# Kernel tuning notes

Measured on AMD Instinct MI355X. Metric: run time of the kernel, lower is better.

## Reference

```python
import jax, jax.numpy as jnp
import numpy as np

FILTER_SIZES = [3, 5, 7, 11, 15, 23, 37, 55]
NB_GROUP = 8
CHAN = 512
IN_CHAN = 3


def setup_inputs() -> dict:
    key = jax.random.key(0)
    keys = jax.random.split(key, 2 + 2 * len(FILTER_SIZES))
    B, H, W = 2, 128, 128
    cpf = CHAN // len(FILTER_SIZES)  # 64 channels per filter size
    inp = {"x": jax.random.normal(keys[0], (B, IN_CHAN, H, W), jnp.float32)}
    for i, k in enumerate(FILTER_SIZES):
        fan_in = IN_CHAN * k * k
        inp[f"w{i}"] = jax.random.normal(keys[1 + 2 * i], (cpf, IN_CHAN, k, k), jnp.float32) / np.sqrt(fan_in).astype(np.float32)
        inp[f"b{i}"] = 0.01 * jax.random.normal(keys[2 + 2 * i], (cpf,), jnp.float32)
    # torch.randperm channel shuffle, fixed for determinism
    inp["perm"] = jax.random.permutation(keys[-1], CHAN)
    return inp


def _conv_relu(x, w, b, k):
    p = (k - 1) // 2  # same padding (odd filter sizes)
    y = jax.lax.conv_general_dilated(
        x, w, window_strides=(1, 1), padding=[(p, p), (p, p)],
        dimension_numbers=("NCHW", "OIHW", "NCHW"))
    return jax.nn.relu(y + b[None, :, None, None])


def reference(x, w0, b0, w1, b1, w2, b2, w3, b3, w4, b4, w5, b5, w6, b6, w7, b7, perm):
    ws = [w0, w1, w2, w3, w4, w5, w6, w7]
    bs = [b0, b1, b2, b3, b4, b5, b6, b7]
    feats = [_conv_relu(x, ws[i], bs[i], FILTER_SIZES[i]) for i in range(len(FILTER_SIZES))]
    feat = jnp.concatenate(feats, axis=1)          # [B, 512, H, W]
    feat = feat[:, perm]                            # channel shuffle
    B, C, H, W = feat.shape
    g = NB_GROUP
    s = C // g
    # unfold(1,s,s)+permute(0,1,4,2,3) == reshape to [B, g, s, H, W]
    feat = feat.reshape(B * g, s, H * W)            # [B*g, s, HW]
    # graham order 2: (feat[:, :, None] * feat[:, None, :]).sum(-1) as a contraction
    gram = jnp.einsum("bcn,bdn->bcd", feat, feat)  # [B*g, s, s]
    return gram.reshape(B, g, s * s)                # [B, g, s*s]
```

## Files before the change

### kernel.cpp

```cpp
#include <hip/hip_runtime.h>
#include <hip/hip_bf16.h>
#include <cstdint>

typedef __attribute__((ext_vector_type(8))) short short8;
typedef __attribute__((ext_vector_type(4))) short short4v;
typedef __attribute__((ext_vector_type(4))) float f32x4;
typedef __attribute__((ext_vector_type(16))) float f32x16;

static constexpr int HWPIX = 16384;
static constexpr int NCH   = 512;
static constexpr int GCHK  = 32;

__device__ __forceinline__ unsigned short f2bf(float f) {
    unsigned int u = __float_as_uint(f);
    u = (u + 0x7fffu + ((u >> 16) & 1u)) >> 16;
    return (unsigned short)u;
}

template<int K> struct KG {
    static constexpr int P       = (K - 1) / 2;
    static constexpr int NSEC    = (K + 7) / 8;
    static constexpr int SEGS    = 3 * K;
    static constexpr int NCHK16  = (SEGS + 1) / 2;
    static constexpr int NCHKP16 = ((NCHK16 + 3) / 4) * 4;
    static constexpr int COLS    = 128 + K - 1;
    static constexpr int XPAD    = 128;
    static constexpr int XSE     = COLS * 24 + XPAD;
};
static_assert(3048 + KG< 3>::NCHKP16 * 16 <= KG< 3>::XSE, "pad3");
static_assert(3048 + KG< 5>::NCHKP16 * 16 <= KG< 5>::XSE, "pad5");
static_assert(3048 + KG< 7>::NCHKP16 * 16 <= KG< 7>::XSE, "pad7");
static_assert(3048 + KG<11>::NCHKP16 * 16 <= KG<11>::XSE, "pad11");
static_assert(3048 + KG<15>::NCHKP16 * 16 <= KG<15>::XSE, "pad15");
static_assert(3048 + KG<23>::NCHKP16 * 16 <= KG<23>::XSE, "pad23");
static_assert(3048 + KG<37>::NCHKP16 * 16 <= KG<37>::XSE, "pad37");
static_assert(3048 + KG<55>::NCHKP16 * 16 <= KG<55>::XSE, "pad55");
static_assert(2 * KG<55>::XSE * 2 <= 33792, "dbuf fits smem");

struct PtrArgs {
    const float* w[8];
    const float* bias[8];
    unsigned short* wpk[8];
    int cum[9];
};

template<int K>
__device__ void repack_body(const float* __restrict__ w, unsigned short* __restrict__ wpk, int t) {
    constexpr int NCHKP16 = KG<K>::NCHKP16;
    const int sec = t / NCHKP16;
    const int t16 = t - sec * NCHKP16;
    const int tid = threadIdx.x;
    if (tid >= 128) return;
    const int strip = tid >> 6;
    const int lane  = tid & 63;
    const int co    = strip * 32 + (lane & 31);
    const int seg   = 2 * t16 + (lane >> 5);
    int kw = 0, r = 0;
    const bool vseg = seg < KG<K>::SEGS;
    if (vseg) { kw = seg / 3; r = seg - kw * 3; }
    short8 o;
    #pragma unroll
    for (int j = 0; j < 8; ++j) {
        const int icr = r * 8 + j;
        const int ic  = icr >> 3;
        const int kh  = sec * 8 + (icr & 7);
        float v = 0.f;
        if (vseg && kh < K)
            v = w[((co * 3 + ic) * K + kh) * K + kw];
        o[j] = (short)f2bf(v);
    }
    *reinterpret_cast<short8*>(wpk + ((size_t)t * 128 + strip * 64 + lane) * 8) = o;
}

__global__ __launch_bounds__(256) void repack_all(PtrArgs a) {
    const int blk = blockIdx.x;
    int f = 0;
    #pragma unroll
    for (int i = 0; i < 8; ++i) if (blk >= a.cum[i + 1]) f = i + 1;
    const int t = blk - a.cum[f];
    switch (f) {
        case 0: repack_body< 3>(a.w[0], a.wpk[0], t); break;
        case 1: repack_body< 5>(a.w[1], a.wpk[1], t); break;
        case 2: repack_body< 7>(a.w[2], a.wpk[2], t); break;
        case 3: repack_body<11>(a.w[3], a.wpk[3], t); break;
        case 4: repack_body<15>(a.w[4], a.wpk[4], t); break;
        case 5: repack_body<23>(a.w[5], a.wpk[5], t); break;
        case 6: repack_body<37>(a.w[6], a.wpk[6], t); break;
        case 7: repack_body<55>(a.w[7], a.wpk[7], t); break;
    }
}

#define MFMA32 __builtin_amdgcn_mfma_f32_32x32x16_bf16

template<int K>
__device__ void conv_body(const float* __restrict__ x, const unsigned short* __restrict__ wpk,
                          const float* __restrict__ bias, unsigned short* __restrict__ feat,
                          int cbase, char* smem, int bx)
{
    constexpr int P        = KG<K>::P;
    constexpr int NCHKP16  = KG<K>::NCHKP16;
    constexpr int NSEC     = KG<K>::NSEC;
    constexpr int COLS     = KG<K>::COLS;
    constexpr int XSE      = KG<K>::XSE;

    unsigned short* xs0 = (unsigned short*)smem;
    float* red = (float*)smem;

    const int tid = threadIdx.x;
    const int b   = bx >> 7;
    const int h   = bx & 127;

    const int lane = tid & 63;
    const int wv   = tid >> 6;
    const int l31  = lane & 31;
    const int lh   = lane >> 5;

    const float* xb = x + (size_t)b * 3 * HWPIX;

    for (int i = tid * 4; i < KG<K>::XPAD; i += 1024) {
        *reinterpret_cast<short4v*>(xs0 + COLS * 24 + i)       = short4v{0, 0, 0, 0};
        *reinterpret_cast<short4v*>(xs0 + XSE + COLS * 24 + i) = short4v{0, 0, 0, 0};
    }

    auto stage = [&](int sec, unsigned short* dst) {
        for (int e = tid * 4; e < 24 * COLS; e += 1024) {
            const int c  = e / 24;
            const int i0 = e - c * 24;
            const int col = c - P;
            short4v pk;
            #pragma unroll
            for (int j = 0; j < 4; ++j) {
                const int icr = i0 + j;
                const int ic  = icr >> 3;
                const int row = h + sec * 8 + (icr & 7) - P;
                float v = 0.f;
                if ((unsigned)row < 128u && (unsigned)col < 128u)
                    v = xb[ic * HWPIX + row * 128 + col];
                pk[j] = (short)f2bf(v);
            }
            *reinterpret_cast<short4v*>(dst + e) = pk;
        }
    };

    stage(0, xs0);
    __syncthreads();

    f32x16 acc[2][4] = {};

    for (int s = 0; s < NSEC; ++s) {
        if (s + 1 < NSEC) stage(s + 1, xs0 + ((s + 1) & 1) * XSE);

        const unsigned short* xsR  = xs0 + (s & 1) * XSE;
        const unsigned short* wsec = wpk + (size_t)s * NCHKP16 * 1024 + lane * 8;

        for (int tt = 0; tt < NCHKP16 / 4; ++tt) {
            const int t16 = tt * 4 + wv;
            const unsigned short* ap = wsec + (size_t)t16 * 1024;
            short8 a0 = *reinterpret_cast<const short8*>(ap);
            short8 a1 = *reinterpret_cast<const short8*>(ap + 512);
            const unsigned short* bp = xsR + l31 * 24 + lh * 8 + t16 * 16;
            short8 b0 = *reinterpret_cast<const short8*>(bp);
            short8 b1 = *reinterpret_cast<const short8*>(bp + 768);
            short8 b2 = *reinterpret_cast<const short8*>(bp + 1536);
            short8 b3 = *reinterpret_cast<const short8*>(bp + 2304);

            acc[0][0] = MFMA32(a0, b0, acc[0][0], 0, 0, 0);
            acc[0][1] = MFMA32(a0, b1, acc[0][1], 0, 0, 0);
            acc[0][2] = MFMA32(a0, b2, acc[0][2], 0, 0, 0);
            acc[0][3] = MFMA32(a0, b3, acc[0][3], 0, 0, 0);
            acc[1][0] = MFMA32(a1, b0, acc[1][0], 0, 0, 0);
            acc[1][1] = MFMA32(a1, b1, acc[1][1], 0, 0, 0);
            acc[1][2] = MFMA32(a1, b2, acc[1][2], 0, 0, 0);
            acc[1][3] = MFMA32(a1, b3, acc[1][3], 0, 0, 0);
        }
        __syncthreads();
    }

    const float bv  = bias[tid >> 2];
    const int   eco = tid >> 2;
    const int   px8 = (tid & 3) * 8;
    const size_t fbase = (((size_t)(b * NCH + cbase + eco)) << 14) + h * 128;

    #pragma unroll
    for (int q = 0; q < 4; ++q) {
        if (q > 0) __syncthreads();
        #pragma unroll
        for (int strip = 0; strip < 2; ++strip)
            #pragma unroll
            for (int reg = 0; reg < 16; ++reg) {
                const int co = strip * 32 + (reg & 3) + 8 * (reg >> 2) + 4 * lh;
                red[(wv * 64 + co) * 33 + l31] = acc[strip][q][reg];
            }
        __syncthreads();
        short8 o;
        #pragma unroll
        for (int j = 0; j < 8; ++j) {
            const int px = px8 + j;
            float v = red[(0 * 64 + eco) * 33 + px] + red[(1 * 64 + eco) * 33 + px]
                    + red[(2 * 64 + eco) * 33 + px] + red[(3 * 64 + eco) * 33 + px];
            o[j] = (short)f2bf(fmaxf(v + bv, 0.f));
        }
        *reinterpret_cast<short8*>(feat + fbase + q * 32 + px8) = o;
    }
}

__global__ __launch_bounds__(256, 2) void conv_all(const float* __restrict__ x,
                                                   PtrArgs a, unsigned short* __restrict__ feat)
{
    __shared__ __align__(16) char smem[33792];
    switch (7 - blockIdx.y) {
        case 0: conv_body< 3>(x, a.wpk[0], a.bias[0], feat, 0 * 64, smem, blockIdx.x); break;
        case 1: conv_body< 5>(x, a.wpk[1], a.bias[1], feat, 1 * 64, smem, blockIdx.x); break;
        case 2: conv_body< 7>(x, a.wpk[2], a.bias[2], feat, 2 * 64, smem, blockIdx.x); break;
        case 3: conv_body<11>(x, a.wpk[3], a.bias[3], feat, 3 * 64, smem, blockIdx.x); break;
        case 4: conv_body<15>(x, a.wpk[4], a.bias[4], feat, 4 * 64, smem, blockIdx.x); break;
        case 5: conv_body<23>(x, a.wpk[5], a.bias[5], feat, 5 * 64, smem, blockIdx.x); break;
        case 6: conv_body<37>(x, a.wpk[6], a.bias[6], feat, 6 * 64, smem, blockIdx.x); break;
        case 7: conv_body<55>(x, a.wpk[7], a.bias[7], feat, 7 * 64, smem, blockIdx.x); break;
    }
}

#define MFMA_BF16 __builtin_amdgcn_mfma_f32_16x16x32_bf16

__global__ __launch_bounds__(256) void gram_mfma(
    const unsigned short* __restrict__ feat, const int* __restrict__ perm,
    float* __restrict__ part)
{
    __shared__ __align__(16) unsigned short tile[64 * 256];
    __shared__ int permch[64];

    const int bg = blockIdx.y, chunk = blockIdx.x;
    const int b = bg >> 3, gq = bg & 7;
    const int tid = threadIdx.x;

    if (tid < 64) permch[tid] = perm[gq * 64 + tid];
    __syncthreads();

    const int lane = tid & 63;
    const int wv   = tid >> 6;
    const int ln15 = lane & 15;
    const int kg   = lane >> 4;

    f32x4 acc[4] = {};
    const size_t pxbase = (size_t)chunk * 512;

    for (int p2 = 0; p2 < 2; ++p2) {
        {
            const int r0 = tid >> 5;
            const int g  = tid & 31;
            #pragma unroll
            for (int it = 0; it < 8; ++it) {
                const int r = it * 8 + r0;
                const unsigned short* src =
                    feat + (((size_t)(b * NCH + permch[r])) << 14) + pxbase + p2 * 256 + g * 8;
                short8 v = *reinterpret_cast<const short8*>(src);
                *reinterpret_cast<short8*>(tile + r * 256 + ((g ^ (r & 7)) * 8)) = v;
            }
        }
        __syncthreads();
        #pragma unroll
        for (int t = 0; t < 8; ++t) {
            const int g  = t * 4 + kg;
            const int ra = wv * 16 + ln15;
            short8 av = *reinterpret_cast<const short8*>(tile + ra * 256 + ((g ^ (ra & 7)) * 8));
            #pragma unroll
            for (int cs = 0; cs < 4; ++cs) {
                const int rb = cs * 16 + ln15;
                short8 bv = *reinterpret_cast<const short8*>(tile + rb * 256 + ((g ^ (rb & 7)) * 8));
                acc[cs] = MFMA_BF16(av, bv, acc[cs], 0, 0, 0);
            }
        }
        __syncthreads();
    }

    float* pp = part + ((size_t)bg * GCHK + chunk) * 4096;
    #pragma unroll
    for (int cs = 0; cs < 4; ++cs)
        #pragma unroll
        for (int i = 0; i < 4; ++i) {
            const int row = wv * 16 + kg * 4 + i;
            const int col = cs * 16 + ln15;
            pp[row * 64 + col] = acc[cs][i];
        }
}

__global__ __launch_bounds__(256) void gram_reduce(
    const float* __restrict__ part, float* __restrict__ out)
{
    const int idx = blockIdx.x * 256 + threadIdx.x;
    const int bg  = idx >> 12;
    const int e   = idx & 4095;
    const float* p = part + (size_t)bg * GCHK * 4096 + e;
    float s = 0.f;
    #pragma unroll
    for (int c = 0; c < GCHK; ++c) s += p[c * 4096];
    out[idx] = s;
}

extern "C" void kernel_launch(void* const* d_in, const int* in_sizes, int n_in,
                              void* d_out, int out_size, void* d_ws, size_t ws_size,
                              hipStream_t stream) {
    const float* x = (const float*)d_in[0];
    const int* perm = (const int*)d_in[17];

    unsigned short* feat = (unsigned short*)d_ws;
    float* part = (float*)((char*)d_ws + (size_t)2 * NCH * HWPIX * sizeof(unsigned short));
    unsigned short* wpk0 = (unsigned short*)((char*)part + (size_t)16 * GCHK * 4096 * sizeof(float));
    float* out = (float*)d_out;

    const int nchk[8] = { KG<3>::NSEC * KG<3>::NCHKP16,  KG<5>::NSEC * KG<5>::NCHKP16,
                          KG<7>::NSEC * KG<7>::NCHKP16,  KG<11>::NSEC * KG<11>::NCHKP16,
                          KG<15>::NSEC * KG<15>::NCHKP16, KG<23>::NSEC * KG<23>::NCHKP16,
                          KG<37>::NSEC * KG<37>::NCHKP16, KG<55>::NSEC * KG<55>::NCHKP16 };
    PtrArgs a;
    int acc = 0;
    for (int i = 0; i < 8; ++i) {
        a.w[i]    = (const float*)d_in[1 + 2 * i];
        a.bias[i] = (const float*)d_in[2 + 2 * i];
        a.wpk[i]  = wpk0 + (size_t)acc * 1024;
        a.cum[i]  = acc;
        acc += nchk[i];
    }
    a.cum[8] = acc;

    repack_all<<<acc, 256, 0, stream>>>(a);
    conv_all<<<dim3(256, 8), 256, 0, stream>>>(x, a, feat);
    gram_mfma<<<dim3(GCHK, 16), 256, 0, stream>>>(feat, perm, part);
    gram_reduce<<<dim3(65536 / 256), 256, 0, stream>>>(part, out);
}
```

Measured before the change: 105.8 us.

## Give each wave private input sections instead of splitting chunks across waves

```diff
diff --git a/kernel.cpp b/kernel.cpp
--- a/kernel.cpp
+++ b/kernel.cpp
@@ -27,15 +27,16 @@
     static constexpr int XPAD    = 128;
     static constexpr int XSE     = COLS * 24 + XPAD;
 };
-static_assert(3048 + KG< 3>::NCHKP16 * 16 <= KG< 3>::XSE, "pad3");
-static_assert(3048 + KG< 5>::NCHKP16 * 16 <= KG< 5>::XSE, "pad5");
-static_assert(3048 + KG< 7>::NCHKP16 * 16 <= KG< 7>::XSE, "pad7");
-static_assert(3048 + KG<11>::NCHKP16 * 16 <= KG<11>::XSE, "pad11");
-static_assert(3048 + KG<15>::NCHKP16 * 16 <= KG<15>::XSE, "pad15");
-static_assert(3048 + KG<23>::NCHKP16 * 16 <= KG<23>::XSE, "pad23");
-static_assert(3048 + KG<37>::NCHKP16 * 16 <= KG<37>::XSE, "pad37");
-static_assert(3048 + KG<55>::NCHKP16 * 16 <= KG<55>::XSE, "pad55");
-static_assert(2 * KG<55>::XSE * 2 <= 33792, "dbuf fits smem");
+static_assert(3048 + KG< 3>::NCHK16 * 16 <= KG< 3>::XSE, "pad3");
+static_assert(3048 + KG< 5>::NCHK16 * 16 <= KG< 5>::XSE, "pad5");
+static_assert(3048 + KG< 7>::NCHK16 * 16 <= KG< 7>::XSE, "pad7");
+static_assert(3048 + KG<11>::NCHK16 * 16 <= KG<11>::XSE, "pad11");
+static_assert(3048 + KG<15>::NCHK16 * 16 <= KG<15>::XSE, "pad15");
+static_assert(3048 + KG<23>::NCHK16 * 16 <= KG<23>::XSE, "pad23");
+static_assert(3048 + KG<37>::NCHK16 * 16 <= KG<37>::XSE, "pad37");
+static_assert(3048 + KG<55>::NCHK16 * 16 <= KG<55>::XSE, "pad55");
+static_assert(4 * KG<55>::XSE * 2 <= 35968, "4 wave buffers fit smem");
+static_assert(256 * 33 * 4 <= 35968, "red fits smem");
 
 struct PtrArgs {
     const float* w[8];
@@ -98,14 +99,12 @@
                           int cbase, char* smem, int bx)
 {
     constexpr int P        = KG<K>::P;
+    constexpr int NCHK16   = KG<K>::NCHK16;
     constexpr int NCHKP16  = KG<K>::NCHKP16;
     constexpr int NSEC     = KG<K>::NSEC;
     constexpr int COLS     = KG<K>::COLS;
     constexpr int XSE      = KG<K>::XSE;
 
-    unsigned short* xs0 = (unsigned short*)smem;
-    float* red = (float*)smem;
-
     const int tid = threadIdx.x;
     const int b   = bx >> 7;
     const int h   = bx & 127;
@@ -115,15 +114,18 @@
     const int l31  = lane & 31;
     const int lh   = lane >> 5;
 
+    unsigned short* xs = (unsigned short*)smem + wv * XSE;
+    float* red = (float*)smem;
+
     const float* xb = x + (size_t)b * 3 * HWPIX;
 
-    for (int i = tid * 4; i < KG<K>::XPAD; i += 1024) {
-        *reinterpret_cast<short4v*>(xs0 + COLS * 24 + i)       = short4v{0, 0, 0, 0};
-        *reinterpret_cast<short4v*>(xs0 + XSE + COLS * 24 + i) = short4v{0, 0, 0, 0};
-    }
-
-    auto stage = [&](int sec, unsigned short* dst) {
-        for (int e = tid * 4; e < 24 * COLS; e += 1024) {
+    for (int i = lane * 4; i < KG<K>::XPAD; i += 256)
+        *reinterpret_cast<short4v*>(xs + COLS * 24 + i) = short4v{0, 0, 0, 0};
+
+    f32x16 acc[2][4] = {};
+
+    for (int s = wv; s < NSEC; s += 4) {
+        for (int e = lane * 4; e < 24 * COLS; e += 256) {
             const int c  = e / 24;
             const int i0 = e - c * 24;
             const int col = c - P;
@@ -132,33 +134,21 @@
             for (int j = 0; j < 4; ++j) {
                 const int icr = i0 + j;
                 const int ic  = icr >> 3;
-                const int row = h + sec * 8 + (icr & 7) - P;
+                const int row = h + s * 8 + (icr & 7) - P;
                 float v = 0.f;
                 if ((unsigned)row < 128u && (unsigned)col < 128u)
                     v = xb[ic * HWPIX + row * 128 + col];
                 pk[j] = (short)f2bf(v);
             }
-            *reinterpret_cast<short4v*>(dst + e) = pk;
-        }
-    };
-
-    stage(0, xs0);
-    __syncthreads();
-
-    f32x16 acc[2][4] = {};
-
-    for (int s = 0; s < NSEC; ++s) {
-        if (s + 1 < NSEC) stage(s + 1, xs0 + ((s + 1) & 1) * XSE);
-
-        const unsigned short* xsR  = xs0 + (s & 1) * XSE;
+            *reinterpret_cast<short4v*>(xs + e) = pk;
+        }
+
         const unsigned short* wsec = wpk + (size_t)s * NCHKP16 * 1024 + lane * 8;
-
-        for (int tt = 0; tt < NCHKP16 / 4; ++tt) {
-            const int t16 = tt * 4 + wv;
+        for (int t16 = 0; t16 < NCHK16; ++t16) {
             const unsigned short* ap = wsec + (size_t)t16 * 1024;
             short8 a0 = *reinterpret_cast<const short8*>(ap);
             short8 a1 = *reinterpret_cast<const short8*>(ap + 512);
-            const unsigned short* bp = xsR + l31 * 24 + lh * 8 + t16 * 16;
+            const unsigned short* bp = xs + l31 * 24 + lh * 8 + t16 * 16;
             short8 b0 = *reinterpret_cast<const short8*>(bp);
             short8 b1 = *reinterpret_cast<const short8*>(bp + 768);
             short8 b2 = *reinterpret_cast<const short8*>(bp + 1536);
@@ -173,9 +163,9 @@
             acc[1][2] = MFMA32(a1, b2, acc[1][2], 0, 0, 0);
             acc[1][3] = MFMA32(a1, b3, acc[1][3], 0, 0, 0);
         }
-        __syncthreads();
-    }
-
+    }
+
+    __syncthreads();
     const float bv  = bias[tid >> 2];
     const int   eco = tid >> 2;
     const int   px8 = (tid & 3) * 8;
@@ -207,7 +197,7 @@
 __global__ __launch_bounds__(256, 2) void conv_all(const float* __restrict__ x,
                                                    PtrArgs a, unsigned short* __restrict__ feat)
 {
-    __shared__ __align__(16) char smem[33792];
+    __shared__ __align__(16) char smem[35968];
     switch (7 - blockIdx.y) {
         case 0: conv_body< 3>(x, a.wpk[0], a.bias[0], feat, 0 * 64, smem, blockIdx.x); break;
         case 1: conv_body< 5>(x, a.wpk[1], a.bias[1], feat, 1 * 64, smem, blockIdx.x); break;
```

Result: slower. 123.0 us (+16.2%).

## Stream conv weight tiles into LDS via async global_load_lds double buffering

Applied to the files above, without the earlier changes.

```diff
diff --git a/kernel.cpp b/kernel.cpp
--- a/kernel.cpp
+++ b/kernel.cpp
@@ -18,24 +18,29 @@
 }
 
 template<int K> struct KG {
-    static constexpr int P       = (K - 1) / 2;
-    static constexpr int NSEC    = (K + 7) / 8;
-    static constexpr int SEGS    = 3 * K;
-    static constexpr int NCHK16  = (SEGS + 1) / 2;
-    static constexpr int NCHKP16 = ((NCHK16 + 3) / 4) * 4;
-    static constexpr int COLS    = 128 + K - 1;
-    static constexpr int XPAD    = 128;
-    static constexpr int XSE     = COLS * 24 + XPAD;
+    static constexpr int P      = (K - 1) / 2;
+    static constexpr int NSEC   = (K + 7) / 8;
+    static constexpr int SEGS   = 3 * K;
+    static constexpr int NCHK16 = (SEGS + 1) / 2;
+    static constexpr int NCHKP8 = ((NCHK16 + 7) / 8) * 8;
+    static constexpr int Q      = NCHKP8 / 4;
+    static constexpr int NP     = Q / 2;
+    static constexpr int COLS   = 128 + K - 1;
+    static constexpr int XPAD   = 128;
+    static constexpr int XSE    = COLS * 24 + XPAD;
 };
-static_assert(3048 + KG< 3>::NCHKP16 * 16 <= KG< 3>::XSE, "pad3");
-static_assert(3048 + KG< 5>::NCHKP16 * 16 <= KG< 5>::XSE, "pad5");
-static_assert(3048 + KG< 7>::NCHKP16 * 16 <= KG< 7>::XSE, "pad7");
-static_assert(3048 + KG<11>::NCHKP16 * 16 <= KG<11>::XSE, "pad11");
-static_assert(3048 + KG<15>::NCHKP16 * 16 <= KG<15>::XSE, "pad15");
-static_assert(3048 + KG<23>::NCHKP16 * 16 <= KG<23>::XSE, "pad23");
-static_assert(3048 + KG<37>::NCHKP16 * 16 <= KG<37>::XSE, "pad37");
-static_assert(3048 + KG<55>::NCHKP16 * 16 <= KG<55>::XSE, "pad55");
-static_assert(2 * KG<55>::XSE * 2 <= 33792, "dbuf fits smem");
+static_assert(3048 + 16 * KG< 3>::NCHKP8 <= KG< 3>::XSE, "pad3");
+static_assert(3048 + 16 * KG< 5>::NCHKP8 <= KG< 5>::XSE, "pad5");
+static_assert(3048 + 16 * KG< 7>::NCHKP8 <= KG< 7>::XSE, "pad7");
+static_assert(3048 + 16 * KG<11>::NCHKP8 <= KG<11>::XSE, "pad11");
+static_assert(3048 + 16 * KG<15>::NCHKP8 <= KG<15>::XSE, "pad15");
+static_assert(3048 + 16 * KG<23>::NCHKP8 <= KG<23>::XSE, "pad23");
+static_assert(3048 + 16 * KG<37>::NCHKP8 <= KG<37>::XSE, "pad37");
+static_assert(3048 + 16 * KG<55>::NCHKP8 <= KG<55>::XSE, "pad55");
+static constexpr int ABYTES = 4 * 2 * 2 * 2048;
+static constexpr int SMEMB  = ABYTES + 2 * KG<55>::XSE * 2;
+static_assert(SMEMB <= 65536, "smem limit");
+static_assert(256 * 33 * 4 <= SMEMB, "red fits");
 
 struct PtrArgs {
     const float* w[8];
@@ -46,9 +51,9 @@
 
 template<int K>
 __device__ void repack_body(const float* __restrict__ w, unsigned short* __restrict__ wpk, int t) {
-    constexpr int NCHKP16 = KG<K>::NCHKP16;
-    const int sec = t / NCHKP16;
-    const int t16 = t - sec * NCHKP16;
+    constexpr int NCHKP8 = KG<K>::NCHKP8;
+    const int sec = t / NCHKP8;
+    const int t16 = t - sec * NCHKP8;
     const int tid = threadIdx.x;
     if (tid >= 128) return;
     const int strip = tid >> 6;
@@ -97,13 +102,16 @@
                           const float* __restrict__ bias, unsigned short* __restrict__ feat,
                           int cbase, char* smem, int bx)
 {
-    constexpr int P        = KG<K>::P;
-    constexpr int NCHKP16  = KG<K>::NCHKP16;
-    constexpr int NSEC     = KG<K>::NSEC;
-    constexpr int COLS     = KG<K>::COLS;
-    constexpr int XSE      = KG<K>::XSE;
-
-    unsigned short* xs0 = (unsigned short*)smem;
+    constexpr int P       = KG<K>::P;
+    constexpr int NCHKP8  = KG<K>::NCHKP8;
+    constexpr int Q       = KG<K>::Q;
+    constexpr int NP      = KG<K>::NP;
+    constexpr int NSEC    = KG<K>::NSEC;
+    constexpr int COLS    = KG<K>::COLS;
+    constexpr int XSE     = KG<K>::XSE;
+
+    unsigned short* aL  = (unsigned short*)smem;
+    unsigned short* xs0 = (unsigned short*)smem + 16384;
     float* red = (float*)smem;
 
     const int tid = threadIdx.x;
@@ -114,6 +122,7 @@
     const int wv   = tid >> 6;
     const int l31  = lane & 31;
     const int lh   = lane >> 5;
+    const int tbase = wv * Q;
 
     const float* xb = x + (size_t)b * 3 * HWPIX;
 
@@ -142,28 +151,30 @@
         }
     };
 
-    stage(0, xs0);
-    __syncthreads();
+    auto glds_phase = [&](int sec, int p) {
+        unsigned short* dst = aL + wv * 4096 + (p & 1) * 2048;
+        const unsigned short* src =
+            wpk + ((size_t)(sec * NCHKP8 + tbase + p * 2) * 128 + lane) * 8;
+        __builtin_amdgcn_global_load_lds((const uint32_t*)(src),        (uint32_t*)(dst),        16, 0, 0);
+        __builtin_amdgcn_global_load_lds((const uint32_t*)(src + 512),  (uint32_t*)(dst + 512),  16, 0, 0);
+        __builtin_amdgcn_global_load_lds((const uint32_t*)(src + 1024), (uint32_t*)(dst + 1024), 16, 0, 0);
+        __builtin_amdgcn_global_load_lds((const uint32_t*)(src + 1536), (uint32_t*)(dst + 1536), 16, 0, 0);
+    };
 
     f32x16 acc[2][4] = {};
 
-    for (int s = 0; s < NSEC; ++s) {
-        if (s + 1 < NSEC) stage(s + 1, xs0 + ((s + 1) & 1) * XSE);
-
-        const unsigned short* xsR  = xs0 + (s & 1) * XSE;
-        const unsigned short* wsec = wpk + (size_t)s * NCHKP16 * 1024 + lane * 8;
-
-        for (int tt = 0; tt < NCHKP16 / 4; ++tt) {
-            const int t16 = tt * 4 + wv;
-            const unsigned short* ap = wsec + (size_t)t16 * 1024;
-            short8 a0 = *reinterpret_cast<const short8*>(ap);
-            short8 a1 = *reinterpret_cast<const short8*>(ap + 512);
+    auto compute = [&](const unsigned short* xsR, int p) {
+        #pragma unroll
+        for (int j = 0; j < 2; ++j) {
+            const int t16 = tbase + p * 2 + j;
+            const unsigned short* ar = aL + wv * 4096 + (p & 1) * 2048 + j * 1024 + lane * 8;
+            short8 a0 = *reinterpret_cast<const short8*>(ar);
+            short8 a1 = *reinterpret_cast<const short8*>(ar + 512);
             const unsigned short* bp = xsR + l31 * 24 + lh * 8 + t16 * 16;
             short8 b0 = *reinterpret_cast<const short8*>(bp);
             short8 b1 = *reinterpret_cast<const short8*>(bp + 768);
             short8 b2 = *reinterpret_cast<const short8*>(bp + 1536);
             short8 b3 = *reinterpret_cast<const short8*>(bp + 2304);
-
             acc[0][0] = MFMA32(a0, b0, acc[0][0], 0, 0, 0);
             acc[0][1] = MFMA32(a0, b1, acc[0][1], 0, 0, 0);
             acc[0][2] = MFMA32(a0, b2, acc[0][2], 0, 0, 0);
@@ -173,6 +184,33 @@
             acc[1][2] = MFMA32(a1, b2, acc[1][2], 0, 0, 0);
             acc[1][3] = MFMA32(a1, b3, acc[1][3], 0, 0, 0);
         }
+    };
+
+    stage(0, xs0);
+    glds_phase(0, 0);
+    if (NP > 1) glds_phase(0, 1);
+    __syncthreads();
+
+    for (int s = 0; s < NSEC; ++s) {
+        if (s + 1 < NSEC) stage(s + 1, xs0 + ((s + 1) & 1) * XSE);
+        const unsigned short* xsR = xs0 + (s & 1) * XSE;
+
+        for (int p = 0; p < NP - 1; ++p) {
+            asm volatile("s_waitcnt vmcnt(4)" ::: "memory");
+            __builtin_amdgcn_sched_barrier(0);
+            compute(xsR, p);
+            __builtin_amdgcn_sched_barrier(0);
+            if (p + 2 < NP) glds_phase(s, p + 2);
+        }
+        asm volatile("s_waitcnt vmcnt(0)" ::: "memory");
+        __builtin_amdgcn_sched_barrier(0);
+        compute(xsR, NP - 1);
+
+        if (s + 1 < NSEC) {
+            __builtin_amdgcn_sched_barrier(0);
+            glds_phase(s + 1, 0);
+            if (NP > 1) glds_phase(s + 1, 1);
+        }
         __syncthreads();
     }
 
@@ -207,7 +245,7 @@
 __global__ __launch_bounds__(256, 2) void conv_all(const float* __restrict__ x,
                                                    PtrArgs a, unsigned short* __restrict__ feat)
 {
-    __shared__ __align__(16) char smem[33792];
+    __shared__ __align__(16) char smem[SMEMB];
     switch (7 - blockIdx.y) {
         case 0: conv_body< 3>(x, a.wpk[0], a.bias[0], feat, 0 * 64, smem, blockIdx.x); break;
         case 1: conv_body< 5>(x, a.wpk[1], a.bias[1], feat, 1 * 64, smem, blockIdx.x); break;
@@ -308,10 +346,10 @@
     unsigned short* wpk0 = (unsigned short*)((char*)part + (size_t)16 * GCHK * 4096 * sizeof(float));
     float* out = (float*)d_out;
 
-    const int nchk[8] = { KG<3>::NSEC * KG<3>::NCHKP16,  KG<5>::NSEC * KG<5>::NCHKP16,
-                          KG<7>::NSEC * KG<7>::NCHKP16,  KG<11>::NSEC * KG<11>::NCHKP16,
-                          KG<15>::NSEC * KG<15>::NCHKP16, KG<23>::NSEC * KG<23>::NCHKP16,
-                          KG<37>::NSEC * KG<37>::NCHKP16, KG<55>::NSEC * KG<55>::NCHKP16 };
+    const int nchk[8] = { KG<3>::NSEC * KG<3>::NCHKP8,  KG<5>::NSEC * KG<5>::NCHKP8,
+                          KG<7>::NSEC * KG<7>::NCHKP8,  KG<11>::NSEC * KG<11>::NCHKP8,
+                          KG<15>::NSEC * KG<15>::NCHKP8, KG<23>::NSEC * KG<23>::NCHKP8,
+                          KG<37>::NSEC * KG<37>::NCHKP8, KG<55>::NSEC * KG<55>::NCHKP8 };
     PtrArgs a;
     int acc = 0;
     for (int i = 0; i < 8; ++i) {
```

Result: slower. 108.9 us (+2.8%).
